# Optimization experiments

Measured on AMD Instinct MI355X. Metric: run time of the kernel, lower is better.

## Reference

```python
import jax, jax.numpy as jnp
import numpy as np

NUM_CLASSES = 19
RMI_RADIUS = 3
POOL_SIZE = 3
POOL_STRIDE = 3
IGNORE_INDEX = 255
LOSS_WEIGHT = 1.0


def _avg_pool_nchw(x, k, s):
    # torch F.avg_pool2d with padding=k//2, count_include_pad=True
    p = k // 2
    summed = jax.lax.reduce_window(
        x, 0.0, jax.lax.add,
        window_dimensions=(1, 1, k, k),
        window_strides=(1, 1, s, s),
        padding=[(0, 0), (0, 0), (p, p), (p, p)])
    return summed / float(k * k)


def _map_get_pairs(labels, probs, radius):
    h, w = labels.shape[2], labels.shape[3]
    nh, nw = h - radius + 1, w - radius + 1
    la = jnp.stack([labels[:, :, y:y + nh, x:x + nw]
                    for y in range(radius) for x in range(radius)], axis=2)
    pr = jnp.stack([probs[:, :, y:y + nh, x:x + nw]
                    for y in range(radius) for x in range(radius)], axis=2)
    return la, pr  # (N, C, r*r, nh, nw)


def _log_det_by_cholesky(mat):
    chol = jnp.linalg.cholesky(mat)
    diag = jnp.diagonal(chol, axis1=-2, axis2=-1)
    return 2.0 * jnp.sum(jnp.log(diag + 1e-8), axis=-1)


def _rmi_lower_bound(labels_4d, probs_4d):
    labels_4d = _avg_pool_nchw(labels_4d, POOL_SIZE, POOL_STRIDE)
    probs_4d = _avg_pool_nchw(probs_4d, POOL_SIZE, POOL_STRIDE)
    la, pr = _map_get_pairs(labels_4d, probs_4d, RMI_RADIUS)
    N, C, D = la.shape[:3]
    la = la.reshape(N, C, D, -1)   # (N, C, D, M)
    pr = pr.reshape(N, C, D, -1)
    M = la.shape[-1]
    la = la - la.mean(axis=-1, keepdims=True)
    pr = pr - pr.mean(axis=-1, keepdims=True)
    la_cov = jnp.einsum('ncdm,ncem->ncde', la, la) / M
    pr_cov = jnp.einsum('ncdm,ncem->ncde', pr, pr) / M
    pr_la_cov = jnp.einsum('ncdm,ncem->ncde', pr, la) / M
    eye = jnp.eye(D, dtype=la_cov.dtype)
    la_cov_inv = jnp.linalg.inv(la_cov + eye * 1e-5)
    appro_var = pr_cov - jnp.einsum('ncde,ncef,ncgf->ncdg',
                                    pr_la_cov, la_cov_inv, pr_la_cov)
    appro_var = appro_var + eye * 1e-6
    rmi_per_class = 0.5 * _log_det_by_cholesky(appro_var)  # (N, C)
    rmi_per_class = rmi_per_class.mean(axis=0)             # (C,)
    return jnp.sum(rmi_per_class) / NUM_CLASSES


def setup_inputs() -> dict:
    key = jax.random.key(0)
    k1, k2 = jax.random.split(key)
    cls_score = jax.random.normal(k1, (4, 19, 512, 512), dtype=jnp.float32)
    label = jax.random.randint(k2, (4, 512, 512), 0, NUM_CLASSES, dtype=jnp.int64)
    return {"cls_score": cls_score, "label": label}


def reference(cls_score, label):
    probs = jax.nn.softmax(cls_score.astype(jnp.float32), axis=1)
    valid = (label >= 0) & (label < NUM_CLASSES) & (label != IGNORE_INDEX)
    lbl = jnp.where(valid, label, 0)
    onehot = jax.nn.one_hot(lbl, NUM_CLASSES, dtype=jnp.float32)
    onehot = jnp.transpose(onehot, (0, 3, 1, 2))  # (N, C, H, W)
    vmask = valid[:, None, :, :].astype(jnp.float32)
    onehot = onehot * vmask
    probs = probs * vmask
    loss = _rmi_lower_bound(onehot, probs)
    return LOSS_WEIGHT * loss
```

## Files before the change

### kernel.cpp

```cpp
#include <hip/hip_runtime.h>
#include <math.h>

#define NBATCH 4
#define NCLS   19
#define HWDIM  512
#define HW     (512 * 512)
#define PH     171
#define PHP    176
#define PP2A   (171 * 176)
#define NHW    169
#define MM     (169 * 169)
#define NBAND  11
#define NSTRIP 43

typedef float f4 __attribute__((ext_vector_type(4)));
typedef float f2 __attribute__((ext_vector_type(2)));

__global__ __launch_bounds__(512) void stage1_pool(
    const float* __restrict__ cls, const int* __restrict__ label,
    float* __restrict__ P, float* __restrict__ L) {
  int n  = blockIdx.x / PH;
  int ph = blockIdx.x - n * PH;
  int col = threadIdx.x;

  float accP[NCLS], accL[NCLS];
#pragma unroll
  for (int c = 0; c < NCLS; ++c) { accP[c] = 0.f; accL[c] = 0.f; }

#pragma unroll
  for (int i = 0; i < 3; ++i) {
    int r = 3 * ph - 1 + i;
    if (r < 0 || r >= HWDIM) continue;
    int lb = label[((size_t)n * HWDIM + r) * HWDIM + col];
    const float* base = cls + (size_t)n * NCLS * HW + (size_t)r * HWDIM + col;
    float v[NCLS];
    float mx = -INFINITY;
#pragma unroll
    for (int c = 0; c < NCLS; ++c) {
      v[c] = base[(size_t)c * HW];
      mx = fmaxf(mx, v[c]);
    }
    float se = 0.f;
#pragma unroll
    for (int c = 0; c < NCLS; ++c) {
      v[c] = expf(v[c] - mx);
      se += v[c];
    }
    if (lb >= 0 && lb < NCLS) {
      float inv = 1.f / se;
#pragma unroll
      for (int c = 0; c < NCLS; ++c) {
        accP[c] += v[c] * inv;
        accL[c] += (lb == c) ? 1.f : 0.f;
      }
    }
  }

  __shared__ float xbP[4][516];
  __shared__ float xbL[4][516];
  const float inv9 = 1.f / 9.f;
#pragma unroll
  for (int c0 = 0; c0 < NCLS; c0 += 4) {
    int nc_round = (NCLS - c0) < 4 ? (NCLS - c0) : 4;
#pragma unroll
    for (int cc = 0; cc < 4; ++cc) {
      if (cc < nc_round) {
        xbP[cc][1 + col] = accP[(c0 + cc) < NCLS ? (c0 + cc) : 0];
        xbL[cc][1 + col] = accL[(c0 + cc) < NCLS ? (c0 + cc) : 0];
        if (col == 0) { xbP[cc][0] = 0.f; xbL[cc][0] = 0.f; }
      }
    }
    __syncthreads();
    if (col < PH) {
      int pw = col;
#pragma unroll
      for (int cc = 0; cc < 4; ++cc) {
        if (cc < nc_round) {
          int c = c0 + cc;
          float sP = xbP[cc][3 * pw] + xbP[cc][3 * pw + 1] + xbP[cc][3 * pw + 2];
          float sL = xbL[cc][3 * pw] + xbL[cc][3 * pw + 1] + xbL[cc][3 * pw + 2];
          size_t o = ((size_t)(n * NCLS + c)) * PP2A + (size_t)ph * PHP + pw;
          P[o] = sP * inv9;
          L[o] = sL * inv9;
        }
      }
    } else if (col < PHP) {
#pragma unroll
      for (int cc = 0; cc < 4; ++cc) {
        if (cc < nc_round) {
          int c = c0 + cc;
          size_t o = ((size_t)(n * NCLS + c)) * PP2A + (size_t)ph * PHP + col;
          P[o] = 0.f;
          L[o] = 0.f;
        }
      }
    }
    __syncthreads();
  }
}

template <int PART>
__device__ __forceinline__ void mom_body(
    const float* __restrict__ Pp, const float* __restrict__ Lp,
    float* __restrict__ covp, int nc, float* red) {
  constexpr int NA  = (PART == 0) ? 63 : (PART == 1 ? 45 : 81);
  constexpr int OFF = (PART == 0) ? 0  : (PART == 1 ? 63 : 108);

  float acc[NA];
#pragma unroll
  for (int k = 0; k < NA; ++k) acc[k] = 0.f;

  int tid = threadIdx.x;
  if (tid < NSTRIP * NBAND) {
    int b  = tid / NSTRIP;
    int s  = tid - b * NSTRIP;
    int x0 = 4 * s;
    int y0 = (NHW * b) / NBAND;
    int y1 = (NHW * (b + 1)) / NBAND;

    float wp[18], wl[18];
#pragma unroll
    for (int r = 0; r < 3; ++r) {
      const float* rp = Pp + (y0 + r) * PHP + x0;
      *(f4*)&wp[r * 6]     = *(const f4*)rp;
      *(f2*)&wp[r * 6 + 4] = *(const f2*)(rp + 4);
      if (PART != 1) {
        const float* rl = Lp + (y0 + r) * PHP + x0;
        *(f4*)&wl[r * 6]     = *(const f4*)rl;
        *(f2*)&wl[r * 6 + 4] = *(const f2*)(rl + 4);
      }
    }

    for (int y = y0; y < y1; ++y) {
      int yn = (y + 3 <= PH - 1) ? (y + 3) : (PH - 1);
      const float* rp = Pp + yn * PHP + x0;
      f4 tp4 = *(const f4*)rp;
      f2 tp2 = *(const f2*)(rp + 4);
      f4 tl4; f2 tl2;
      if (PART != 1) {
        const float* rl = Lp + yn * PHP + x0;
        tl4 = *(const f4*)rl;
        tl2 = *(const f2*)(rl + 4);
      }
#pragma unroll
      for (int p = 0; p < 4; ++p) {
        if (x0 + p < NHW) {
          if (PART == 0) {
#pragma unroll
            for (int dy = 0; dy < 3; ++dy)
#pragma unroll
              for (int dx = 0; dx < 3; ++dx) {
                int d = dy * 3 + dx;
                acc[d]     += wl[dy * 6 + p + dx];
                acc[9 + d] += wp[dy * 6 + p + dx];
              }
            int k = 18;
#pragma unroll
            for (int d = 0; d < 9; ++d)
#pragma unroll
              for (int e = d; e < 9; ++e) {
                acc[k] += wl[(d / 3) * 6 + p + (d % 3)] *
                          wl[(e / 3) * 6 + p + (e % 3)];
                ++k;
              }
          } else if (PART == 1) {
            int k = 0;
#pragma unroll
            for (int d = 0; d < 9; ++d)
#pragma unroll
              for (int e = d; e < 9; ++e) {
                acc[k] += wp[(d / 3) * 6 + p + (d % 3)] *
                          wp[(e / 3) * 6 + p + (e % 3)];
                ++k;
              }
          } else {
#pragma unroll
            for (int d = 0; d < 9; ++d)
#pragma unroll
              for (int e = 0; e < 9; ++e)
                acc[d * 9 + e] += wp[(d / 3) * 6 + p + (d % 3)] *
                                  wl[(e / 3) * 6 + p + (e % 3)];
          }
        }
      }
#pragma unroll
      for (int t = 0; t < 12; ++t) {
        wp[t] = wp[t + 6];
        if (PART != 1) wl[t] = wl[t + 6];
      }
      *(f4*)&wp[12] = tp4;
      *(f2*)&wp[16] = tp2;
      if (PART != 1) {
        *(f4*)&wl[12] = tl4;
        *(f2*)&wl[16] = tl2;
      }
    }
  }

  int lane = threadIdx.x & 63;
  int wid  = threadIdx.x >> 6;
#pragma unroll
  for (int k = 0; k < NA; ++k) {
    float v = acc[k];
#pragma unroll
    for (int o = 32; o > 0; o >>= 1) v += __shfl_down(v, o, 64);
    if (lane == 0) red[wid * NA + k] = v;
  }
  __syncthreads();
  if (threadIdx.x < NA) {
    float sm = 0.f;
#pragma unroll
    for (int w = 0; w < 8; ++w) sm += red[w * NA + threadIdx.x];
    covp[(size_t)nc * 192 + OFF + threadIdx.x] = sm;
  }
}

__global__ __launch_bounds__(512) void stage2_mom(
    const float* __restrict__ P, const float* __restrict__ L,
    float* __restrict__ covp) {
  __shared__ float red[8 * 81];
  int nc = blockIdx.x;
  const float* Pp = P + (size_t)nc * PP2A;
  const float* Lp = L + (size_t)nc * PP2A;
  if (blockIdx.y == 0)      mom_body<0>(Pp, Lp, covp, nc, red);
  else if (blockIdx.y == 1) mom_body<1>(Pp, Lp, covp, nc, red);
  else                      mom_body<2>(Pp, Lp, covp, nc, red);
}

__global__ __launch_bounds__(64) void stage3_rmi(float* __restrict__ covp) {
  int nc  = blockIdx.x;
  int tid = threadIdx.x;
  const float* s = covp + (size_t)nc * 192;
  __shared__ double lc[81], pc[81], plc[81], mla[9], mpr[9];
  const double Minv = 1.0 / (double)MM;

  if (tid < 9)       mla[tid]     = (double)s[tid] * Minv;
  else if (tid < 18) mpr[tid - 9] = (double)s[tid] * Minv;
  __syncthreads();

  for (int e = tid; e < 81; e += 64) {
    int r = e / 9, c = e - 9 * (e / 9);
    int lo = r < c ? r : c, hi = r < c ? c : r;
    int k = lo * 9 - lo * (lo - 1) / 2 + (hi - lo);
    double a = (double)s[18 + k] * Minv - mla[r] * mla[c];
    if (r == c) a += 1e-5;
    lc[e] = a;
    pc[e] = (double)s[63 + k] * Minv - mpr[r] * mpr[c];
    plc[e] = (double)s[108 + e] * Minv - mpr[r] * mla[c];
  }
  __syncthreads();

  for (int j = 0; j < 9; ++j) {
    if (tid == 0) lc[j * 9 + j] = sqrt(lc[j * 9 + j]);
    __syncthreads();
    if (tid > j && tid < 9) lc[tid * 9 + j] /= lc[j * 9 + j];
    __syncthreads();
    if (tid > j && tid < 9) {
      double lij = lc[tid * 9 + j];
      for (int k = j + 1; k <= tid; ++k) lc[tid * 9 + k] -= lij * lc[k * 9 + j];
    }
    __syncthreads();
  }

  if (tid < 9) {
    int d = tid;
    for (int j = 0; j < 9; ++j) {
      double t = plc[d * 9 + j];
      for (int k = 0; k < j; ++k) t -= plc[d * 9 + k] * lc[j * 9 + k];
      plc[d * 9 + j] = t / lc[j * 9 + j];
    }
  }
  __syncthreads();

  for (int e = tid; e < 81; e += 64) {
    int r = e / 9, c = e - 9 * (e / 9);
    double a = pc[e];
    for (int f = 0; f < 9; ++f) a -= plc[r * 9 + f] * plc[c * 9 + f];
    if (r == c) a += 1e-6;
    pc[e] = a;
  }
  __syncthreads();

  for (int j = 0; j < 9; ++j) {
    if (tid == 0) pc[j * 9 + j] = sqrt(pc[j * 9 + j]);
    __syncthreads();
    if (tid > j && tid < 9) pc[tid * 9 + j] /= pc[j * 9 + j];
    __syncthreads();
    if (tid > j && tid < 9) {
      double lij = pc[tid * 9 + j];
      for (int k = j + 1; k <= tid; ++k) pc[tid * 9 + k] -= lij * pc[k * 9 + j];
    }
    __syncthreads();
  }

  if (tid == 0) {
    double sl = 0.0;
    for (int j = 0; j < 9; ++j) sl += log(pc[j * 9 + j] + 1e-8);
    *(double*)(covp + (size_t)nc * 192 + 190) = sl;
  }
}

__global__ __launch_bounds__(64) void stage4_reduce(
    const float* __restrict__ covp, float* __restrict__ out) {
  int tid = threadIdx.x;
  double v = 0.0;
  if (tid < NBATCH * NCLS)
    v = *(const double*)(covp + (size_t)tid * 192 + 190);
  if (tid + 64 < NBATCH * NCLS)
    v += *(const double*)(covp + (size_t)(tid + 64) * 192 + 190);
#pragma unroll
  for (int o = 32; o > 0; o >>= 1) v += __shfl_down(v, o, 64);
  if (tid == 0) out[0] = (float)(v / (double)(NBATCH * NCLS));
}

extern "C" void kernel_launch(void* const* d_in, const int* in_sizes, int n_in,
                              void* d_out, int out_size, void* d_ws, size_t ws_size,
                              hipStream_t stream) {
  const float* cls  = (const float*)d_in[0];
  const int* label  = (const int*)d_in[1];
  float* out = (float*)d_out;

  float* P    = (float*)d_ws;
  float* L    = P + (size_t)NBATCH * NCLS * PP2A;
  float* covp = L + (size_t)NBATCH * NCLS * PP2A;

  stage1_pool<<<NBATCH * PH, 512, 0, stream>>>(cls, label, P, L);
  dim3 g2(NBATCH * NCLS, 3, 1);
  stage2_mom<<<g2, 512, 0, stream>>>(P, L, covp);
  stage3_rmi<<<NBATCH * NCLS, 64, 0, stream>>>(covp);
  stage4_reduce<<<1, 64, 0, stream>>>(covp, out);
}
```

Measured before the change: 76.56 us.

## Split moment rows across z-blocks, hoist loads and specialize interior strips

Stage 2 now splits the row range into two z-slices, doubling the block count, and writes partial moment records that stage 3 sums in double. Interior column strips get a branch-free 4-position path and the cross-wave reduction is shortened to three shuffles plus a larger shared-memory sum. Stage 1 issues all three rows' loads before the softmax, uses __expf, masks invalid pixels arithmetically and processes ten classes per shared-memory round. The changes trade extra shared memory, register pressure and partial-record traffic for more parallelism and memory-level concurrency.

After: 85.61 us. +11.8%, slower.

```diff
diff --git a/kernel.cpp b/kernel.cpp
--- a/kernel.cpp
+++ b/kernel.cpp
@@ -12,6 +12,7 @@
 #define MM     (169 * 169)
 #define NBAND  11
 #define NSTRIP 43
+#define ZS     2
 
 typedef float f4 __attribute__((ext_vector_type(4)));
 typedef float f2 __attribute__((ext_vector_type(2)));
@@ -23,48 +24,57 @@
   int ph = blockIdx.x - n * PH;
   int col = threadIdx.x;
 
-  float accP[NCLS], accL[NCLS];
-#pragma unroll
-  for (int c = 0; c < NCLS; ++c) { accP[c] = 0.f; accL[c] = 0.f; }
-
+  float vv[3][NCLS];
+  int lbs[3];
 #pragma unroll
   for (int i = 0; i < 3; ++i) {
     int r = 3 * ph - 1 + i;
-    if (r < 0 || r >= HWDIM) continue;
-    int lb = label[((size_t)n * HWDIM + r) * HWDIM + col];
-    const float* base = cls + (size_t)n * NCLS * HW + (size_t)r * HWDIM + col;
-    float v[NCLS];
-    float mx = -INFINITY;
+    bool ok = (r >= 0) && (r < HWDIM);
+    if (ok) {
+      lbs[i] = label[((size_t)n * HWDIM + r) * HWDIM + col];
+      const float* base = cls + (size_t)n * NCLS * HW + (size_t)r * HWDIM + col;
+#pragma unroll
+      for (int c = 0; c < NCLS; ++c) vv[i][c] = base[(size_t)c * HW];
+    } else {
+      lbs[i] = -1;
+#pragma unroll
+      for (int c = 0; c < NCLS; ++c) vv[i][c] = 0.f;
+    }
+  }
+
+  float accP[NCLS], accL[NCLS];
+#pragma unroll
+  for (int c = 0; c < NCLS; ++c) { accP[c] = 0.f; accL[c] = 0.f; }
+#pragma unroll
+  for (int i = 0; i < 3; ++i) {
+    int lb = lbs[i];
+    float mx = vv[i][0];
+#pragma unroll
+    for (int c = 1; c < NCLS; ++c) mx = fmaxf(mx, vv[i][c]);
+    float se = 0.f;
+    float ex[NCLS];
 #pragma unroll
     for (int c = 0; c < NCLS; ++c) {
-      v[c] = base[(size_t)c * HW];
-      mx = fmaxf(mx, v[c]);
-    }
-    float se = 0.f;
+      ex[c] = __expf(vv[i][c] - mx);
+      se += ex[c];
+    }
+    float m = (lb >= 0 && lb < NCLS) ? 1.f : 0.f;
+    float inv = m / se;
 #pragma unroll
     for (int c = 0; c < NCLS; ++c) {
-      v[c] = expf(v[c] - mx);
-      se += v[c];
-    }
-    if (lb >= 0 && lb < NCLS) {
-      float inv = 1.f / se;
-#pragma unroll
-      for (int c = 0; c < NCLS; ++c) {
-        accP[c] += v[c] * inv;
-        accL[c] += (lb == c) ? 1.f : 0.f;
-      }
-    }
-  }
-
-  __shared__ float xbP[4][516];
-  __shared__ float xbL[4][516];
+      accP[c] += ex[c] * inv;
+      accL[c] += (lb == c) ? 1.f : 0.f;
+    }
+  }
+
+  __shared__ float xbP[10][516];
+  __shared__ float xbL[10][516];
   const float inv9 = 1.f / 9.f;
 #pragma unroll
-  for (int c0 = 0; c0 < NCLS; c0 += 4) {
-    int nc_round = (NCLS - c0) < 4 ? (NCLS - c0) : 4;
-#pragma unroll
-    for (int cc = 0; cc < 4; ++cc) {
-      if (cc < nc_round) {
+  for (int c0 = 0; c0 < NCLS; c0 += 10) {
+#pragma unroll
+    for (int cc = 0; cc < 10; ++cc) {
+      if (c0 + cc < NCLS) {
         xbP[cc][1 + col] = accP[(c0 + cc) < NCLS ? (c0 + cc) : 0];
         xbL[cc][1 + col] = accL[(c0 + cc) < NCLS ? (c0 + cc) : 0];
         if (col == 0) { xbP[cc][0] = 0.f; xbL[cc][0] = 0.f; }
@@ -74,8 +84,8 @@
     if (col < PH) {
       int pw = col;
 #pragma unroll
-      for (int cc = 0; cc < 4; ++cc) {
-        if (cc < nc_round) {
+      for (int cc = 0; cc < 10; ++cc) {
+        if (c0 + cc < NCLS) {
           int c = c0 + cc;
           float sP = xbP[cc][3 * pw] + xbP[cc][3 * pw + 1] + xbP[cc][3 * pw + 2];
           float sL = xbL[cc][3 * pw] + xbL[cc][3 * pw + 1] + xbL[cc][3 * pw + 2];
@@ -86,8 +96,8 @@
       }
     } else if (col < PHP) {
 #pragma unroll
-      for (int cc = 0; cc < 4; ++cc) {
-        if (cc < nc_round) {
+      for (int cc = 0; cc < 10; ++cc) {
+        if (c0 + cc < NCLS) {
           int c = c0 + cc;
           size_t o = ((size_t)(n * NCLS + c)) * PP2A + (size_t)ph * PHP + col;
           P[o] = 0.f;
@@ -99,10 +109,49 @@
   }
 }
 
+template <int PART, int NA, int POS>
+__device__ __forceinline__ void fma_pos(float (&acc)[NA],
+                                        const float (&wp)[18],
+                                        const float (&wl)[18]) {
+  if (PART == 0) {
+#pragma unroll
+    for (int d = 0; d < 9; ++d) {
+      acc[d]     += wl[(d / 3) * 6 + POS + (d % 3)];
+      acc[9 + d] += wp[(d / 3) * 6 + POS + (d % 3)];
+    }
+    int k = 18;
+#pragma unroll
+    for (int d = 0; d < 9; ++d)
+#pragma unroll
+      for (int e = d; e < 9; ++e) {
+        acc[k] += wl[(d / 3) * 6 + POS + (d % 3)] *
+                  wl[(e / 3) * 6 + POS + (e % 3)];
+        ++k;
+      }
+  } else if (PART == 1) {
+    int k = 0;
+#pragma unroll
+    for (int d = 0; d < 9; ++d)
+#pragma unroll
+      for (int e = d; e < 9; ++e) {
+        acc[k] += wp[(d / 3) * 6 + POS + (d % 3)] *
+                  wp[(e / 3) * 6 + POS + (e % 3)];
+        ++k;
+      }
+  } else {
+#pragma unroll
+    for (int d = 0; d < 9; ++d)
+#pragma unroll
+      for (int e = 0; e < 9; ++e)
+        acc[d * 9 + e] += wp[(d / 3) * 6 + POS + (d % 3)] *
+                          wl[(e / 3) * 6 + POS + (e % 3)];
+  }
+}
+
 template <int PART>
 __device__ __forceinline__ void mom_body(
     const float* __restrict__ Pp, const float* __restrict__ Lp,
-    float* __restrict__ covp, int nc, float* red) {
+    float* __restrict__ covp, int rec, int z, float* red) {
   constexpr int NA  = (PART == 0) ? 63 : (PART == 1 ? 45 : 81);
   constexpr int OFF = (PART == 0) ? 0  : (PART == 1 ? 63 : 108);
 
@@ -115,8 +164,11 @@
     int b  = tid / NSTRIP;
     int s  = tid - b * NSTRIP;
     int x0 = 4 * s;
-    int y0 = (NHW * b) / NBAND;
-    int y1 = (NHW * (b + 1)) / NBAND;
+    int zr0 = (NHW * z) / ZS;
+    int zr1 = (NHW * (z + 1)) / ZS;
+    int zr  = zr1 - zr0;
+    int y0 = zr0 + (zr * b) / NBAND;
+    int y1 = zr0 + (zr * (b + 1)) / NBAND;
 
     float wp[18], wl[18];
 #pragma unroll
@@ -131,68 +183,52 @@
       }
     }
 
-    for (int y = y0; y < y1; ++y) {
-      int yn = (y + 3 <= PH - 1) ? (y + 3) : (PH - 1);
-      const float* rp = Pp + yn * PHP + x0;
-      f4 tp4 = *(const f4*)rp;
-      f2 tp2 = *(const f2*)(rp + 4);
-      f4 tl4; f2 tl2;
-      if (PART != 1) {
-        const float* rl = Lp + yn * PHP + x0;
-        tl4 = *(const f4*)rl;
-        tl2 = *(const f2*)(rl + 4);
-      }
-#pragma unroll
-      for (int p = 0; p < 4; ++p) {
-        if (x0 + p < NHW) {
-          if (PART == 0) {
-#pragma unroll
-            for (int dy = 0; dy < 3; ++dy)
-#pragma unroll
-              for (int dx = 0; dx < 3; ++dx) {
-                int d = dy * 3 + dx;
-                acc[d]     += wl[dy * 6 + p + dx];
-                acc[9 + d] += wp[dy * 6 + p + dx];
-              }
-            int k = 18;
-#pragma unroll
-            for (int d = 0; d < 9; ++d)
-#pragma unroll
-              for (int e = d; e < 9; ++e) {
-                acc[k] += wl[(d / 3) * 6 + p + (d % 3)] *
-                          wl[(e / 3) * 6 + p + (e % 3)];
-                ++k;
-              }
-          } else if (PART == 1) {
-            int k = 0;
-#pragma unroll
-            for (int d = 0; d < 9; ++d)
-#pragma unroll
-              for (int e = d; e < 9; ++e) {
-                acc[k] += wp[(d / 3) * 6 + p + (d % 3)] *
-                          wp[(e / 3) * 6 + p + (e % 3)];
-                ++k;
-              }
-          } else {
-#pragma unroll
-            for (int d = 0; d < 9; ++d)
-#pragma unroll
-              for (int e = 0; e < 9; ++e)
-                acc[d * 9 + e] += wp[(d / 3) * 6 + p + (d % 3)] *
-                                  wl[(e / 3) * 6 + p + (e % 3)];
-          }
-        }
-      }
-#pragma unroll
-      for (int t = 0; t < 12; ++t) {
-        wp[t] = wp[t + 6];
-        if (PART != 1) wl[t] = wl[t + 6];
-      }
-      *(f4*)&wp[12] = tp4;
-      *(f2*)&wp[16] = tp2;
-      if (PART != 1) {
-        *(f4*)&wl[12] = tl4;
-        *(f2*)&wl[16] = tl2;
+    if (x0 + 4 <= NHW) {
+      for (int y = y0; y < y1; ++y) {
+        int yn = (y + 3 <= PH - 1) ? (y + 3) : (PH - 1);
+        const float* rp = Pp + yn * PHP + x0;
+        f4 tp4 = *(const f4*)rp;
+        f2 tp2 = *(const f2*)(rp + 4);
+        f4 tl4; f2 tl2;
+        if (PART != 1) {
+          const float* rl = Lp + yn * PHP + x0;
+          tl4 = *(const f4*)rl;
+          tl2 = *(const f2*)(rl + 4);
+        }
+        fma_pos<PART, NA, 0>(acc, wp, wl);
+        fma_pos<PART, NA, 1>(acc, wp, wl);
+        fma_pos<PART, NA, 2>(acc, wp, wl);
+        fma_pos<PART, NA, 3>(acc, wp, wl);
+#pragma unroll
+        for (int t = 0; t < 12; ++t) {
+          wp[t] = wp[t + 6];
+          if (PART != 1) wl[t] = wl[t + 6];
+        }
+        *(f4*)&wp[12] = tp4;
+        *(f2*)&wp[16] = tp2;
+        if (PART != 1) { *(f4*)&wl[12] = tl4; *(f2*)&wl[16] = tl2; }
+      }
+    } else {
+      for (int y = y0; y < y1; ++y) {
+        int yn = (y + 3 <= PH - 1) ? (y + 3) : (PH - 1);
+        const float* rp = Pp + yn * PHP + x0;
+        f4 tp4 = *(const f4*)rp;
+        f2 tp2 = *(const f2*)(rp + 4);
+        f4 tl4; f2 tl2;
+        if (PART != 1) {
+          const float* rl = Lp + yn * PHP + x0;
+          tl4 = *(const f4*)rl;
+          tl2 = *(const f2*)(rl + 4);
+        }
+        fma_pos<PART, NA, 0>(acc, wp, wl);
+#pragma unroll
+        for (int t = 0; t < 12; ++t) {
+          wp[t] = wp[t + 6];
+          if (PART != 1) wl[t] = wl[t + 6];
+        }
+        *(f4*)&wp[12] = tp4;
+        *(f2*)&wp[16] = tp2;
+        if (PART != 1) { *(f4*)&wl[12] = tl4; *(f2*)&wl[16] = tl2; }
       }
     }
   }
@@ -202,51 +238,56 @@
 #pragma unroll
   for (int k = 0; k < NA; ++k) {
     float v = acc[k];
-#pragma unroll
-    for (int o = 32; o > 0; o >>= 1) v += __shfl_down(v, o, 64);
-    if (lane == 0) red[wid * NA + k] = v;
-  }
-  __syncthreads();
-  if (threadIdx.x < NA) {
+    v += __shfl_down(v, 32, 64);
+    v += __shfl_down(v, 16, 64);
+    v += __shfl_down(v, 8, 64);
+    if (lane < 8) red[(wid * 8 + lane) * 84 + k] = v;
+  }
+  __syncthreads();
+  if (tid < NA) {
     float sm = 0.f;
 #pragma unroll
-    for (int w = 0; w < 8; ++w) sm += red[w * NA + threadIdx.x];
-    covp[(size_t)nc * 192 + OFF + threadIdx.x] = sm;
+    for (int w = 0; w < 64; ++w) sm += red[w * 84 + tid];
+    covp[(size_t)rec * 192 + OFF + tid] = sm;
   }
 }
 
 __global__ __launch_bounds__(512) void stage2_mom(
     const float* __restrict__ P, const float* __restrict__ L,
     float* __restrict__ covp) {
-  __shared__ float red[8 * 81];
+  __shared__ float red[64 * 84];
   int nc = blockIdx.x;
+  int z  = blockIdx.z;
+  int rec = z * (NBATCH * NCLS) + nc;
   const float* Pp = P + (size_t)nc * PP2A;
   const float* Lp = L + (size_t)nc * PP2A;
-  if (blockIdx.y == 0)      mom_body<0>(Pp, Lp, covp, nc, red);
-  else if (blockIdx.y == 1) mom_body<1>(Pp, Lp, covp, nc, red);
-  else                      mom_body<2>(Pp, Lp, covp, nc, red);
+  if (blockIdx.y == 0)      mom_body<0>(Pp, Lp, covp, rec, z, red);
+  else if (blockIdx.y == 1) mom_body<1>(Pp, Lp, covp, rec, z, red);
+  else                      mom_body<2>(Pp, Lp, covp, rec, z, red);
 }
 
 __global__ __launch_bounds__(64) void stage3_rmi(float* __restrict__ covp) {
   int nc  = blockIdx.x;
   int tid = threadIdx.x;
-  const float* s = covp + (size_t)nc * 192;
+  const float* s0 = covp + (size_t)nc * 192;
+  const float* s1 = covp + ((size_t)NBATCH * NCLS + nc) * 192;
   __shared__ double lc[81], pc[81], plc[81], mla[9], mpr[9];
   const double Minv = 1.0 / (double)MM;
-
-  if (tid < 9)       mla[tid]     = (double)s[tid] * Minv;
-  else if (tid < 18) mpr[tid - 9] = (double)s[tid] * Minv;
+#define LDM(k) ((double)s0[k] + (double)s1[k])
+
+  if (tid < 9)       mla[tid]     = LDM(tid) * Minv;
+  else if (tid < 18) mpr[tid - 9] = LDM(tid) * Minv;
   __syncthreads();
 
   for (int e = tid; e < 81; e += 64) {
     int r = e / 9, c = e - 9 * (e / 9);
     int lo = r < c ? r : c, hi = r < c ? c : r;
     int k = lo * 9 - lo * (lo - 1) / 2 + (hi - lo);
-    double a = (double)s[18 + k] * Minv - mla[r] * mla[c];
+    double a = LDM(18 + k) * Minv - mla[r] * mla[c];
     if (r == c) a += 1e-5;
     lc[e] = a;
-    pc[e] = (double)s[63 + k] * Minv - mpr[r] * mpr[c];
-    plc[e] = (double)s[108 + e] * Minv - mpr[r] * mla[c];
+    pc[e] = LDM(63 + k) * Minv - mpr[r] * mpr[c];
+    plc[e] = LDM(108 + e) * Minv - mpr[r] * mla[c];
   }
   __syncthreads();
 
@@ -298,6 +339,7 @@
     for (int j = 0; j < 9; ++j) sl += log(pc[j * 9 + j] + 1e-8);
     *(double*)(covp + (size_t)nc * 192 + 190) = sl;
   }
+#undef LDM
 }
 
 __global__ __launch_bounds__(64) void stage4_reduce(
@@ -325,7 +367,7 @@
   float* covp = L + (size_t)NBATCH * NCLS * PP2A;
 
   stage1_pool<<<NBATCH * PH, 512, 0, stream>>>(cls, label, P, L);
-  dim3 g2(NBATCH * NCLS, 3, 1);
+  dim3 g2(NBATCH * NCLS, 3, ZS);
   stage2_mom<<<g2, 512, 0, stream>>>(P, L, covp);
   stage3_rmi<<<NBATCH * NCLS, 64, 0, stream>>>(covp);
   stage4_reduce<<<1, 64, 0, stream>>>(covp, out);
```
